# Optimization experiments

Measured on AMD Instinct MI355X. Metric: run time of the kernel, lower is better.

## Reference

```python
import jax, jax.numpy as jnp
import numpy as np

V, L, NP, NC, D, S, NNEG = 2, 2, 120000, 120000, 128, 100, 50
TEMP = 0.5


def setup_inputs() -> dict:
    key = jax.random.key(0)
    ks = jax.random.split(key, 10)
    return {
        'emb_p': jax.random.normal(ks[0], (V, L, NP, D), dtype=jnp.float32),
        'emb_c': jax.random.normal(ks[1], (V, L, NC, D), dtype=jnp.float32),
        'W1': jax.random.normal(ks[2], (D, D), dtype=jnp.float32) * (1.0 / np.sqrt(D)),
        'b1': jax.random.normal(ks[3], (D,), dtype=jnp.float32) * 0.01,
        'W2': jax.random.normal(ks[4], (D, D), dtype=jnp.float32) * (1.0 / np.sqrt(D)),
        'b2': jax.random.normal(ks[5], (D,), dtype=jnp.float32) * 0.01,
        'idx_p': jax.random.randint(ks[6], (V, L, S), 0, NP, dtype=jnp.int64),
        'idx_c': jax.random.randint(ks[7], (V, L, S), 0, NC, dtype=jnp.int64),
        'neg_idx_p': jax.random.randint(ks[8], (V, L, S, NNEG), 0, NC, dtype=jnp.int64),
        'neg_idx_c': jax.random.randint(ks[9], (V, L, S, NNEG), 0, NP, dtype=jnp.int64),
    }


def _l2norm(x):
    return x / jnp.maximum(jnp.linalg.norm(x, axis=-1, keepdims=True), 1e-12)


def _type_loss(Pz_self, Pz_other, idx, neg_idx):
    total = jnp.float32(0.0)
    for vi in range(V):
        for li in range(L):
            ids = idx[vi, li]                      # [S]
            z = Pz_self[vi, li][ids]               # [S,D] anchor projections
            # positives: same node index, all other (view,layer) keys (3 when V=L=2)
            pos_keys = [(1 - vi, li), (vi, 1 - li), (1 - vi, 1 - li)]
            pos = jnp.stack([Pz_self[vj, lj][ids] for vj, lj in pos_keys])  # [3,S,D]
            pos_sim = jnp.exp(jnp.einsum('sd,ksd->ks', z, pos) / TEMP).sum(0)  # [S]
            # within-type negatives: other sampled anchors (exclude self position)
            sims = jnp.exp(z @ z.T / TEMP)         # [S,S]
            neg_within = sims.sum(1) - jnp.diagonal(sims)
            # cross-type negatives: 50 sampled per anchor from other type, same key
            ng = Pz_other[vi, li][neg_idx[vi, li]]  # [S,NNEG,D]
            neg_cross = jnp.exp(jnp.einsum('sd,snd->sn', z, ng) / TEMP).sum(1)
            neg = neg_within + neg_cross
            total = total + (-jnp.log(pos_sim / (pos_sim + neg))).sum()
    return total


def reference(emb_p, emb_c, W1, b1, W2, b2, idx_p, idx_c, neg_idx_p, neg_idx_c):
    def project(x):
        return jnp.maximum(x @ W1 + b1, 0.0) @ W2 + b2
    Pz_p = _l2norm(project(emb_p))  # [V,L,NP,D]
    Pz_c = _l2norm(project(emb_c))  # [V,L,NC,D]
    total = _type_loss(Pz_p, Pz_c, idx_p, neg_idx_p) + _type_loss(Pz_c, Pz_p, idx_c, neg_idx_c)
    total_samples = 2 * V * L * S
    return total / jnp.float32(total_samples)
```

## Files before the change

### kernel.cpp

```cpp
#include <hip/hip_runtime.h>
#include <hip/hip_bf16.h>
#include <math.h>

#define NNODE 120000
#define DDIM  128
#define SS    100
#define NNEGS 50
#define ROWS_A 1600
#define ROWS_N 20000
#define TOTAL_ROWS 43200
#define BLK_ROWS 256
#define NBLK 169
#define INV_TEMP 2.0f

typedef unsigned short ushort_t;
typedef __attribute__((ext_vector_type(8))) short bf16x8;
typedef __attribute__((ext_vector_type(8))) unsigned short u16x8;
typedef __attribute__((ext_vector_type(4))) float f32x4;

__device__ __forceinline__ ushort_t f2b(float f) {
  __hip_bfloat16 h = __float2bfloat16(f);
  return *reinterpret_cast<ushort_t*>(&h);
}
__device__ __forceinline__ float b2f(ushort_t h) {
  return __builtin_bit_cast(float, (unsigned)h << 16);
}
__device__ __forceinline__ bool idx_is64(const void* p) {
  const unsigned* q = (const unsigned*)p;
  return (q[1] | q[3] | q[5] | q[7]) == 0u;
}
__device__ __forceinline__ int ld_idx(const void* p, int i, bool is64) {
  return is64 ? (int)((const long long*)p)[i] : ((const int*)p)[i];
}

__device__ __forceinline__ const float* row_src(
    int rid, bool is64,
    const float* emb_p, const float* emb_c,
    const void* idx_p, const void* idx_c,
    const void* nidx_p, const void* nidx_c)
{
  if (rid < 2 * ROWS_A) {
    const int typ = rid / ROWS_A;
    const int rr  = rid - typ * ROWS_A;
    const int slice = rr / 400;
    const int rem   = rr - slice * 400;
    const int node  = ld_idx(typ ? idx_c : idx_p, rem, is64);
    return (typ ? emb_c : emb_p) + ((size_t)slice * NNODE + node) * DDIM;
  } else {
    const int r2  = rid - 2 * ROWS_A;
    const int typ = r2 / ROWS_N;
    const int rr  = r2 - typ * ROWS_N;
    const int slice = rr / (SS * NNEGS);
    const int rem   = rr - slice * (SS * NNEGS);
    const int node  = ld_idx(typ ? nidx_c : nidx_p, slice * (SS * NNEGS) + rem, is64);
    return (typ ? emb_p : emb_c) + ((size_t)slice * NNODE + node) * DDIM;
  }
}

__global__ __launch_bounds__(512, 2)
void proj_kernel(const float* __restrict__ emb_p, const float* __restrict__ emb_c,
                 const float* __restrict__ W1, const float* __restrict__ b1v,
                 const float* __restrict__ W2, const float* __restrict__ b2v,
                 const void* __restrict__ idx_p, const void* __restrict__ idx_c,
                 const void* __restrict__ nidx_p, const void* __restrict__ nidx_c,
                 ushort_t* __restrict__ zout, float* __restrict__ out)
{
  __shared__ __align__(16) ushort_t wlds[2 * 16384];
  __shared__ __align__(16) ushort_t slab[BLK_ROWS * DDIM];
  const int t = threadIdx.x, w = t >> 6, l = t & 63;
  const int g = l >> 4, li = l & 15;
  const bool is64 = idx_is64(idx_p);
  const int base = blockIdx.x * BLK_ROWS;
  const int ra = w * 32 + li;
  const int rb = ra + 16;
  char* hb = (char*)slab;

  if (blockIdx.x == 0 && t == 0) out[0] = 0.f;

  int rida = base + ra, ridb = base + rb;
  if (rida > TOTAL_ROWS - 1) rida = TOTAL_ROWS - 1;
  if (ridb > TOTAL_ROWS - 1) ridb = TOTAL_ROWS - 1;
  const float* sa = row_src(rida, is64, emb_p, emb_c, idx_p, idx_c, nidx_p, nidx_c);
  const float* sb = row_src(ridb, is64, emb_p, emb_c, idx_p, idx_c, nidx_p, nidx_c);
  bf16x8 afa[4], afb[4];
  #pragma unroll
  for (int kc = 0; kc < 4; ++kc) {
    const float4 a0 = *(const float4*)(sa + kc * 32 + g * 8);
    const float4 a1 = *(const float4*)(sa + kc * 32 + g * 8 + 4);
    const float4 b0 = *(const float4*)(sb + kc * 32 + g * 8);
    const float4 b1 = *(const float4*)(sb + kc * 32 + g * 8 + 4);
    bf16x8 fa, fb;
    fa[0]=(short)f2b(a0.x); fa[1]=(short)f2b(a0.y); fa[2]=(short)f2b(a0.z); fa[3]=(short)f2b(a0.w);
    fa[4]=(short)f2b(a1.x); fa[5]=(short)f2b(a1.y); fa[6]=(short)f2b(a1.z); fa[7]=(short)f2b(a1.w);
    fb[0]=(short)f2b(b0.x); fb[1]=(short)f2b(b0.y); fb[2]=(short)f2b(b0.z); fb[3]=(short)f2b(b0.w);
    fb[4]=(short)f2b(b1.x); fb[5]=(short)f2b(b1.y); fb[6]=(short)f2b(b1.z); fb[7]=(short)f2b(b1.w);
    afa[kc] = fa; afb[kc] = fb;
  }

  #pragma unroll
  for (int p = 0; p < 8; ++p) {
    const int s = p * 512 + t;
    const int layer = s >> 11;
    const int idx = s & 2047;
    const int lane = idx & 63, kcct = idx >> 6;
    const int kc = kcct >> 3, ct = kcct & 7;
    const float* W = layer ? W2 : W1;
    const float* wp = W + (size_t)(kc * 32 + ((lane >> 4) << 3)) * DDIM
                        + ct * 16 + (lane & 15);
    u16x8 v;
    #pragma unroll
    for (int e = 0; e < 8; ++e) v[e] = f2b(wp[(size_t)e * DDIM]);
    *(u16x8*)&wlds[(size_t)s * 8] = v;
  }
  __syncthreads();

  f32x4 aa[8], ab[8];
  #pragma unroll
  for (int ct = 0; ct < 8; ++ct) {
    const float bv = b1v[ct * 16 + li];
    aa[ct] = (f32x4){bv, bv, bv, bv};
    ab[ct] = aa[ct];
  }
  #pragma unroll
  for (int kc = 0; kc < 4; ++kc)
    #pragma unroll
    for (int ct = 0; ct < 8; ++ct) {
      const bf16x8 bf = *(const bf16x8*)&wlds[((kc * 8 + ct) * 64 + l) * 8];
      aa[ct] = __builtin_amdgcn_mfma_f32_16x16x32_bf16(afa[kc], bf, aa[ct], 0, 0, 0);
      ab[ct] = __builtin_amdgcn_mfma_f32_16x16x32_bf16(afb[kc], bf, ab[ct], 0, 0, 0);
    }
  #pragma unroll
  for (int ct = 0; ct < 8; ++ct)
    #pragma unroll
    for (int rg = 0; rg < 4; ++rg) {
      const int rowa = w * 32 + 4 * g + rg;
      const int bytea = rowa * 256 + (ct * 16 + li) * 2;
      *(ushort_t*)(hb + (bytea ^ ((rowa & 7) << 4))) = f2b(fmaxf(aa[ct][rg], 0.f));
      const int rowb = rowa + 16;
      const int byteb = rowb * 256 + (ct * 16 + li) * 2;
      *(ushort_t*)(hb + (byteb ^ ((rowb & 7) << 4))) = f2b(fmaxf(ab[ct][rg], 0.f));
    }
  #pragma unroll
  for (int ct = 0; ct < 8; ++ct) {
    const float bv = b2v[ct * 16 + li];
    aa[ct] = (f32x4){bv, bv, bv, bv};
    ab[ct] = aa[ct];
  }
  #pragma unroll
  for (int kc = 0; kc < 4; ++kc) {
    const int rowa = w * 32 + li, rowb = rowa + 16;
    const int bytea = rowa * 256 + kc * 64 + g * 16;
    const int byteb = rowb * 256 + kc * 64 + g * 16;
    const bf16x8 hfa = *(const bf16x8*)(hb + (bytea ^ ((rowa & 7) << 4)));
    const bf16x8 hfb = *(const bf16x8*)(hb + (byteb ^ ((rowb & 7) << 4)));
    #pragma unroll
    for (int ct = 0; ct < 8; ++ct) {
      const bf16x8 bf = *(const bf16x8*)&wlds[16384 + ((kc * 8 + ct) * 64 + l) * 8];
      aa[ct] = __builtin_amdgcn_mfma_f32_16x16x32_bf16(hfa, bf, aa[ct], 0, 0, 0);
      ab[ct] = __builtin_amdgcn_mfma_f32_16x16x32_bf16(hfb, bf, ab[ct], 0, 0, 0);
    }
  }
  #pragma unroll
  for (int grp = 0; grp < 2; ++grp) {
    f32x4* ac = grp ? ab : aa;
    float sc[4];
    #pragma unroll
    for (int rg = 0; rg < 4; ++rg) {
      float ssq = 0.f;
      #pragma unroll
      for (int ct = 0; ct < 8; ++ct) ssq += ac[ct][rg] * ac[ct][rg];
      ssq += __shfl_xor(ssq, 1);
      ssq += __shfl_xor(ssq, 2);
      ssq += __shfl_xor(ssq, 4);
      ssq += __shfl_xor(ssq, 8);
      sc[rg] = 1.f / fmaxf(sqrtf(ssq), 1e-12f);
    }
    #pragma unroll
    for (int ct = 0; ct < 8; ++ct)
      #pragma unroll
      for (int rg = 0; rg < 4; ++rg)
        slab[(w * 32 + grp * 16 + 4 * g + rg) * DDIM + ct * 16 + li] =
            f2b(ac[ct][rg] * sc[rg]);
  }
  {
    const uint4* s4 = (const uint4*)&slab[(w * 32) * DDIM];
    uint4* d4 = (uint4*)(zout + (size_t)(base + w * 32) * DDIM);
    #pragma unroll
    for (int i = 0; i < 8; ++i) d4[l + 64 * i] = s4[l + 64 * i];
  }
}

__global__ __launch_bounds__(256)
void loss_kernel(const ushort_t* __restrict__ zb, float* __restrict__ out)
{
  __shared__ float sp[4], sn[4];
  const int bid = blockIdx.x;
  const int grp = bid & 7;
  const int s   = bid >> 3;
  const int typ = grp >> 2;
  const int vl  = grp & 3;
  const ushort_t* A  = zb + (size_t)(typ ? ROWS_A : 0) * DDIM;
  const ushort_t* Nb = zb + (size_t)(2 * ROWS_A + (typ ? ROWS_N : 0)) * DDIM;
  const ushort_t* zs = A + (size_t)((vl * 4 + vl) * SS + s) * DDIM;
  const int t = threadIdx.x, l = t & 63, w = t >> 6;
  const int tsub = l >> 3, eg = l & 7;

  float zr[16];
  {
    const u16x8 v0 = *(const u16x8*)(zs + eg * 16);
    const u16x8 v1 = *(const u16x8*)(zs + eg * 16 + 8);
    #pragma unroll
    for (int j = 0; j < 8; ++j) { zr[j] = b2f(v0[j]); zr[j + 8] = b2f(v1[j]); }
  }

  float pe = 0.f, ne = 0.f;
  #pragma unroll
  for (int pass = 0; pass < 5; ++pass) {
    const int tt = pass * 32 + w * 8 + tsub;
    float d = 0.f;
    bool act = (tt < 152);
    if (act) {
      const ushort_t* tp;
      if (tt < 3) {
        const int k = tt + (tt >= vl ? 1 : 0);
        tp = A + (size_t)((k * 4 + vl) * SS + s) * DDIM;
      } else if (tt < 102) {
        int t2 = tt - 3;
        if (t2 >= s) ++t2;
        tp = A + (size_t)((vl * 4 + vl) * SS + t2) * DDIM;
      } else {
        tp = Nb + (size_t)((vl * SS + s) * NNEGS + (tt - 102)) * DDIM;
      }
      const u16x8 x0 = *(const u16x8*)(tp + eg * 16);
      const u16x8 x1 = *(const u16x8*)(tp + eg * 16 + 8);
      #pragma unroll
      for (int j = 0; j < 8; ++j) {
        d = fmaf(b2f(x0[j]), zr[j], d);
        d = fmaf(b2f(x1[j]), zr[j + 8], d);
      }
    }
    d += __shfl_xor(d, 1);
    d += __shfl_xor(d, 2);
    d += __shfl_xor(d, 4);
    const float e = act ? __expf(d * INV_TEMP) : 0.f;
    if (tt < 3) pe += e; else ne += e;
  }
  pe += __shfl_xor(pe, 8);  ne += __shfl_xor(ne, 8);
  pe += __shfl_xor(pe, 16); ne += __shfl_xor(ne, 16);
  pe += __shfl_xor(pe, 32); ne += __shfl_xor(ne, 32);
  if (l == 0) { sp[w] = pe; sn[w] = ne; }
  __syncthreads();
  if (t == 0) {
    const float P  = sp[0] + sp[1] + sp[2] + sp[3];
    const float Ng = sn[0] + sn[1] + sn[2] + sn[3];
    atomicAdd(out, -logf(P / (P + Ng)) * (1.0f / 800.0f));
  }
}

extern "C" void kernel_launch(void* const* d_in, const int* in_sizes, int n_in,
                              void* d_out, int out_size, void* d_ws, size_t ws_size,
                              hipStream_t stream) {
  const float* emb_p = (const float*)d_in[0];
  const float* emb_c = (const float*)d_in[1];
  const float* W1    = (const float*)d_in[2];
  const float* b1    = (const float*)d_in[3];
  const float* W2    = (const float*)d_in[4];
  const float* b2    = (const float*)d_in[5];
  const void*  idx_p  = d_in[6];
  const void*  idx_c  = d_in[7];
  const void*  nidx_p = d_in[8];
  const void*  nidx_c = d_in[9];
  float* out = (float*)d_out;
  ushort_t* zrows = (ushort_t*)d_ws;

  proj_kernel<<<NBLK, 512, 0, stream>>>(
      emb_p, emb_c, W1, b1, W2, b2, idx_p, idx_c, nidx_p, nidx_c, zrows, out);
  loss_kernel<<<800, 256, 0, stream>>>(zrows, out);
}
```

Measured before the change: 34.82 us.

## Restructure loss kernel: one wave per anchor, stage anchor slab in LDS

```diff
diff --git a/kernel.cpp b/kernel.cpp
--- a/kernel.cpp
+++ b/kernel.cpp
@@ -190,21 +190,34 @@
   }
 }
 
-__global__ __launch_bounds__(256)
+#define LROW_U4 17
+__global__ __launch_bounds__(512)
 void loss_kernel(const ushort_t* __restrict__ zb, float* __restrict__ out)
 {
-  __shared__ float sp[4], sn[4];
+  __shared__ __align__(16) uint4 sl[SS * LROW_U4];
+  __shared__ float sterm[8];
   const int bid = blockIdx.x;
   const int grp = bid & 7;
-  const int s   = bid >> 3;
+  const int chunk = bid >> 3;
   const int typ = grp >> 2;
   const int vl  = grp & 3;
   const ushort_t* A  = zb + (size_t)(typ ? ROWS_A : 0) * DDIM;
   const ushort_t* Nb = zb + (size_t)(2 * ROWS_A + (typ ? ROWS_N : 0)) * DDIM;
-  const ushort_t* zs = A + (size_t)((vl * 4 + vl) * SS + s) * DDIM;
+  const ushort_t* SL = A + (size_t)(vl * 4 + vl) * SS * DDIM;
   const int t = threadIdx.x, l = t & 63, w = t >> 6;
   const int tsub = l >> 3, eg = l & 7;
-
+  const int s_raw = chunk * 8 + w;
+  const bool act = (s_raw < SS);
+  const int s = act ? s_raw : SS - 1;
+
+  #pragma unroll
+  for (int i = 0; i < 4; ++i) {
+    const int c = i * 512 + t;
+    if (c < SS * 16)
+      sl[(c >> 4) * LROW_U4 + (c & 15)] = ((const uint4*)SL)[c];
+  }
+
+  const ushort_t* zs = SL + (size_t)s * DDIM;
   float zr[16];
   {
     const u16x8 v0 = *(const u16x8*)(zs + eg * 16);
@@ -215,45 +228,74 @@
 
   float pe = 0.f, ne = 0.f;
   #pragma unroll
-  for (int pass = 0; pass < 5; ++pass) {
-    const int tt = pass * 32 + w * 8 + tsub;
+  for (int pass = 0; pass < 6; ++pass) {
+    const int n = pass * 8 + tsub;
+    const ushort_t* tp = Nb + (size_t)((vl * SS + s) * NNEGS + n) * DDIM;
+    const u16x8 x0 = *(const u16x8*)(tp + eg * 16);
+    const u16x8 x1 = *(const u16x8*)(tp + eg * 16 + 8);
     float d = 0.f;
-    bool act = (tt < 152);
-    if (act) {
+    #pragma unroll
+    for (int j = 0; j < 8; ++j) {
+      d = fmaf(b2f(x0[j]), zr[j], d);
+      d = fmaf(b2f(x1[j]), zr[j + 8], d);
+    }
+    d += __shfl_xor(d, 1);
+    d += __shfl_xor(d, 2);
+    d += __shfl_xor(d, 4);
+    ne += __expf(d * INV_TEMP);
+  }
+  __syncthreads();
+
+  #pragma unroll
+  for (int pass = 6; pass < 19; ++pass) {
+    const int tt = pass * 8 + tsub;
+    float d = 0.f;
+    bool is_pos = false;
+    if (tt >= 53) {
+      int j = tt - 53;
+      int t2 = j + (j >= s ? 1 : 0);
+      const uint4* rp = &sl[t2 * LROW_U4 + eg * 2];
+      const u16x8 x0 = *(const u16x8*)rp;
+      const u16x8 x1 = *(const u16x8*)(rp + 1);
+      #pragma unroll
+      for (int j2 = 0; j2 < 8; ++j2) {
+        d = fmaf(b2f(x0[j2]), zr[j2], d);
+        d = fmaf(b2f(x1[j2]), zr[j2 + 8], d);
+      }
+    } else {
       const ushort_t* tp;
-      if (tt < 3) {
-        const int k = tt + (tt >= vl ? 1 : 0);
+      if (tt < 50) {
+        tp = Nb + (size_t)((vl * SS + s) * NNEGS + tt) * DDIM;
+      } else {
+        const int kp = tt - 50;
+        const int k = kp + (kp >= vl ? 1 : 0);
         tp = A + (size_t)((k * 4 + vl) * SS + s) * DDIM;
-      } else if (tt < 102) {
-        int t2 = tt - 3;
-        if (t2 >= s) ++t2;
-        tp = A + (size_t)((vl * 4 + vl) * SS + t2) * DDIM;
-      } else {
-        tp = Nb + (size_t)((vl * SS + s) * NNEGS + (tt - 102)) * DDIM;
+        is_pos = true;
       }
       const u16x8 x0 = *(const u16x8*)(tp + eg * 16);
       const u16x8 x1 = *(const u16x8*)(tp + eg * 16 + 8);
       #pragma unroll
-      for (int j = 0; j < 8; ++j) {
-        d = fmaf(b2f(x0[j]), zr[j], d);
-        d = fmaf(b2f(x1[j]), zr[j + 8], d);
+      for (int j2 = 0; j2 < 8; ++j2) {
+        d = fmaf(b2f(x0[j2]), zr[j2], d);
+        d = fmaf(b2f(x1[j2]), zr[j2 + 8], d);
       }
     }
     d += __shfl_xor(d, 1);
     d += __shfl_xor(d, 2);
     d += __shfl_xor(d, 4);
-    const float e = act ? __expf(d * INV_TEMP) : 0.f;
-    if (tt < 3) pe += e; else ne += e;
+    const float e = __expf(d * INV_TEMP);
+    if (is_pos) pe += e; else ne += e;
   }
   pe += __shfl_xor(pe, 8);  ne += __shfl_xor(ne, 8);
   pe += __shfl_xor(pe, 16); ne += __shfl_xor(ne, 16);
   pe += __shfl_xor(pe, 32); ne += __shfl_xor(ne, 32);
-  if (l == 0) { sp[w] = pe; sn[w] = ne; }
+  if (l == 0) sterm[w] = act ? -logf(pe / (pe + ne)) : 0.f;
   __syncthreads();
   if (t == 0) {
-    const float P  = sp[0] + sp[1] + sp[2] + sp[3];
-    const float Ng = sn[0] + sn[1] + sn[2] + sn[3];
-    atomicAdd(out, -logf(P / (P + Ng)) * (1.0f / 800.0f));
+    float tot = 0.f;
+    #pragma unroll
+    for (int i = 0; i < 8; ++i) tot += sterm[i];
+    atomicAdd(out, tot * (1.0f / 800.0f));
   }
 }
 
@@ -275,5 +317,5 @@
 
   proj_kernel<<<NBLK, 512, 0, stream>>>(
       emb_p, emb_c, W1, b1, W2, b2, idx_p, idx_c, nidx_p, nidx_c, zrows, out);
-  loss_kernel<<<800, 256, 0, stream>>>(zrows, out);
-}
+  loss_kernel<<<104, 512, 0, stream>>>(zrows, out);
+}
```

New measurement: 28.37 us. 18.5% less time.
